# Kernel tuning notes

Hardware: AMD Instinct MI355X
Metric: run time of the kernel (lower is better)

Reference implementation:

```python
import jax, jax.numpy as jnp
import numpy as np

VAR0, VAR1 = 0.1, 0.2
THRESHOLD = 0.35
NEGPOS_RATIO = 7
LOW_GT_THRESH = 0.2  # match() filters GT whose best prior IoU < 0.2


def setup_inputs() -> dict:
    key = jax.random.key(0)
    ks = jax.random.split(key, 8)
    B, P, G = 16, 43008, 128
    loc_data = jax.random.normal(ks[0], (B, P, 4), jnp.float32)
    conf_data = jax.random.normal(ks[1], (B, P, 2), jnp.float32)
    landm_data = jax.random.normal(ks[2], (B, P, 10), jnp.float32)
    # priors in cxcywh form, positive sizes
    pc = jax.random.uniform(ks[3], (P, 2), jnp.float32)
    pwh = jax.random.uniform(ks[4], (P, 2), jnp.float32, minval=0.02, maxval=0.32)
    priors = jnp.concatenate([pc, pwh], axis=1)
    # targets: valid xyxy boxes + 10 landmark coords + label (face=1)
    ctr = jax.random.uniform(ks[5], (B, G, 2), jnp.float32, minval=0.2, maxval=0.8)
    wh = jax.random.uniform(ks[6], (B, G, 2), jnp.float32, minval=0.05, maxval=0.3)
    boxes = jnp.concatenate([ctr - wh / 2, ctr + wh / 2], axis=-1)
    landms = jax.random.uniform(ks[7], (B, G, 10), jnp.float32)
    labels = jnp.ones((B, G, 1), jnp.float32)
    targets = jnp.concatenate([boxes, landms, labels], axis=-1)
    return {"loc_data": loc_data, "conf_data": conf_data, "landm_data": landm_data,
            "priors": priors, "targets": targets}


def point_form(priors):
    return jnp.concatenate([priors[:, :2] - priors[:, 2:] / 2,
                            priors[:, :2] + priors[:, 2:] / 2], axis=1)


def jaccard(a, b):  # a: [G,4] xyxy, b: [P,4] xyxy -> [G,P]
    lt = jnp.maximum(a[:, None, :2], b[None, :, :2])
    rb = jnp.minimum(a[:, None, 2:], b[None, :, 2:])
    wh = jnp.clip(rb - lt, 0.0)
    inter = wh[..., 0] * wh[..., 1]
    area_a = (a[:, 2] - a[:, 0]) * (a[:, 3] - a[:, 1])
    area_b = (b[:, 2] - b[:, 0]) * (b[:, 3] - b[:, 1])
    return inter / (area_a[:, None] + area_b[None, :] - inter)


def encode(matched, priors):  # matched xyxy [P,4], priors cxcywh [P,4]
    g_cxcy = (matched[:, :2] + matched[:, 2:]) / 2 - priors[:, :2]
    g_cxcy = g_cxcy / (VAR0 * priors[:, 2:])
    g_wh = jnp.log((matched[:, 2:] - matched[:, :2]) / priors[:, 2:]) / VAR1
    return jnp.concatenate([g_cxcy, g_wh], axis=1)


def encode_landm(matched, priors):  # matched [P,10], priors [P,4]
    m = matched.reshape(-1, 5, 2)
    g = (m - priors[:, None, :2]) / (VAR0 * priors[:, None, 2:])
    return g.reshape(-1, 10)


def match_one(truths, labels, landms, priors):
    G = truths.shape[0]
    overlaps = jaccard(truths, point_form(priors))  # [G, P]
    best_prior_overlap = overlaps.max(axis=1)       # [G]
    best_prior_idx = overlaps.argmax(axis=1)        # [G]
    valid = best_prior_overlap >= LOW_GT_THRESH
    any_valid = jnp.any(valid)
    best_truth_overlap = overlaps.max(axis=0)       # [P]
    best_truth_idx = overlaps.argmax(axis=0)        # [P]
    # index_fill_(0, best_prior_idx_filter, 2): ensure each valid GT keeps its best prior
    fill_val = jnp.where(valid, 2.0, best_truth_overlap[best_prior_idx])
    best_truth_overlap = best_truth_overlap.at[best_prior_idx].set(fill_val)
    # best_truth_idx[best_prior_idx[j]] = j for all j
    best_truth_idx = best_truth_idx.at[best_prior_idx].set(jnp.arange(G))
    matches = truths[best_truth_idx]                       # [P,4]
    conf = labels[best_truth_idx].astype(jnp.int32)        # [P]
    conf = jnp.where(best_truth_overlap < THRESHOLD, 0, conf)
    conf = jnp.where(any_valid, conf, 0)  # no valid GT -> all background
    loc = encode(matches, priors)
    landm = encode_landm(landms[best_truth_idx], priors)
    return loc, conf, landm


def smooth_l1(x):
    ax = jnp.abs(x)
    return jnp.where(ax < 1.0, 0.5 * ax * ax, ax - 0.5)


def reference(loc_data, conf_data, landm_data, priors, targets):
    truths = targets[..., :4]
    landms = targets[..., 4:14]
    labels = targets[..., 14]
    loc_t, conf_t, landm_t = jax.vmap(
        lambda t, l, lm: match_one(t, l, lm, priors))(truths, labels, landms)

    # landmark loss over positives
    pos1 = conf_t > 0
    N1 = jnp.maximum(pos1.sum().astype(jnp.float32), 1.0)
    loss_landm = jnp.sum(smooth_l1(landm_data - landm_t) * pos1[..., None])

    # localization loss over positives
    pos = conf_t != 0
    num_pos = pos.sum(axis=1, keepdims=True)  # [B,1]
    loss_l = jnp.sum(smooth_l1(loc_data - loc_t) * pos[..., None])

    # hard negative mining on per-prior CE loss
    lse = jax.scipy.special.logsumexp(conf_data, axis=-1)  # [B,P]
    gathered = jnp.take_along_axis(conf_data, conf_t[..., None], axis=-1)[..., 0]
    ce_all = lse - gathered                                # [B,P] per-prior CE
    mine = jnp.where(pos, 0.0, ce_all)
    loss_idx = jnp.argsort(-mine, axis=1)
    idx_rank = jnp.argsort(loss_idx, axis=1)
    num_neg = jnp.clip(NEGPOS_RATIO * num_pos, None, pos.shape[1] - 1)
    neg = idx_rank < num_neg
    sel = pos | neg
    loss_c = jnp.sum(jnp.where(sel, ce_all, 0.0))

    N = jnp.maximum(num_pos.sum().astype(jnp.float32), 1.0)
    return loss_l / N, loss_c / N, loss_landm / N1
```

## Files before the change

kernel.cpp:

```cpp
#include <hip/hip_runtime.h>
#include <stdint.h>


#define GC 8
#define PPI 4

__device__ __forceinline__ float sl1(float x) {
  float a = fabsf(x);
  return a < 1.f ? 0.5f * a * a : a - 0.5f;
}

__device__ __forceinline__ double dwave(double v) {
#pragma unroll
  for (int o = 32; o; o >>= 1) v += __shfl_down(v, o);
  return v;
}

__global__ __launch_bounds__(256) void k_mm(
    const float* __restrict__ priors, const float* __restrict__ targets,
    const float* __restrict__ loc, const float* __restrict__ conf,
    const float* __restrict__ lm, float* __restrict__ bto,
    int* __restrict__ bti, unsigned long long* __restrict__ bp,
    float* __restrict__ mine, unsigned* __restrict__ ghist,
    double* __restrict__ pll, double* __restrict__ pllm,
    double* __restrict__ plc, double* __restrict__ msum,
    int* __restrict__ pnp, int P, int G, int NIOU, int PTI, int NGC, int PC) {
  int tid = threadIdx.x;
  __shared__ char smem[16384];
  __shared__ float4 sgt[128];
  __shared__ float sga[128];

  if ((int)blockIdx.x < NIOU) {
    float* st = (float*)smem;
    double* rs = (double*)(smem + 7680);
    int* ri = (int*)(smem + 7808);
    unsigned* hist = (unsigned*)(smem + 8192);
    int b = blockIdx.x / PTI, tile = blockIdx.x % PTI;
    int base = tile * (256 * PPI);
    for (int i = tid; i < G * 15; i += 256)
      st[i] = targets[(size_t)b * G * 15 + i];
    for (int g = tid; g < G; g += 256) {
      const float* t = targets + ((size_t)b * G + g) * 15;
      float x1 = t[0], y1 = t[1], x2 = t[2], y2 = t[3];
      sgt[g] = make_float4(x1, y1, x2, y2);
      sga[g] = (x2 - x1) * (y2 - y1);
    }
    for (int i = tid; i < 1024; i += 256) hist[i] = 0;
    __syncthreads();

    float px1[PPI], py1[PPI], px2[PPI], py2[PPI], pa[PPI];
    float bi[PPI], sb[PPI];
    int bidx[PPI];
#pragma unroll
    for (int k = 0; k < PPI; ++k) {
      int p = base + tid + k * 256;
      int pl = p < P ? p : P - 1;
      float4 pr = ((const float4*)priors)[pl];
      px1[k] = pr.x - pr.z * 0.5f; py1[k] = pr.y - pr.w * 0.5f;
      px2[k] = pr.x + pr.z * 0.5f; py2[k] = pr.y + pr.w * 0.5f;
      pa[k] = pr.z * pr.w;
      bi[k] = 0.f; sb[k] = 1.f; bidx[k] = 0;
    }

#define IOU_BODY(T, A, GG)                                                 \
  {                                                                        \
    float iw = fminf(T.z, px2[k]) - fmaxf(T.x, px1[k]);                    \
    float ih = fminf(T.w, py2[k]) - fmaxf(T.y, py1[k]);                    \
    float inter = fmaxf(iw, 0.f) * ih;                                     \
    float S = A + pa[k];                                                   \
    if (inter * sb[k] > bi[k] * S) { bi[k] = inter; sb[k] = S; bidx[k] = GG; } \
  }
    for (int g = 0; g < G; g += 4) {
      float4 T0 = sgt[g], T1 = sgt[g + 1], T2 = sgt[g + 2], T3 = sgt[g + 3];
      float A0 = sga[g], A1 = sga[g + 1], A2 = sga[g + 2], A3 = sga[g + 3];
#pragma unroll
      for (int k = 0; k < PPI; ++k) {
        IOU_BODY(T0, A0, g)
        IOU_BODY(T1, A1, g + 1)
        IOU_BODY(T2, A2, g + 2)
        IOU_BODY(T3, A3, g + 3)
      }
    }
#undef IOU_BODY

    double ll = 0, llm = 0, lc = 0, ms = 0;
    int np = 0;
#pragma unroll
    for (int k = 0; k < PPI; ++k) {
      int p = base + tid + k * 256;
      if (p < P) {
        size_t idx = (size_t)b * P + p;
        float ov = bi[k] / (sb[k] - bi[k]);
        int ti = bidx[k];
        bto[idx] = ov;
        bti[idx] = ti;
        bool pos = ov >= 0.35f;
        float2 c = ((const float2*)conf)[idx];
        float mx = fmaxf(c.x, c.y);
        float dd = fabsf(c.x - c.y);
        float lse = mx + logf(1.f + expf(-dd));
        float ce = lse - (pos ? c.y : c.x);
        float mv = pos ? 0.f : ce;
        mine[idx] = mv;
        atomicAdd(&hist[__float_as_uint(mv) >> 21], 1u);
        ms += (double)mv;
        if (pos) {
          np++;
          lc += (double)ce;
          float4 pr = ((const float4*)priors)[p];
          const float* t = st + ti * 15;
          float rz = 1.f / pr.z, rw = 1.f / pr.w;
          float rdx = 10.f * rz, rdy = 10.f * rw;
          float gx = ((t[0] + t[2]) * 0.5f - pr.x) * rdx;
          float gy = ((t[1] + t[3]) * 0.5f - pr.y) * rdy;
          float gw = logf((t[2] - t[0]) * rz) * 5.0f;
          float gh = logf((t[3] - t[1]) * rw) * 5.0f;
          float4 ld = ((const float4*)loc)[idx];
          ll += (double)(sl1(ld.x - gx) + sl1(ld.y - gy) + sl1(ld.z - gw) +
                         sl1(ld.w - gh));
          const float2* lmd = (const float2*)lm + idx * 5;
          float s = 0.f;
#pragma unroll
          for (int j = 0; j < 5; ++j) {
            float2 lv = lmd[j];
            float ex = (t[4 + 2 * j] - pr.x) * rdx;
            float ey = (t[5 + 2 * j] - pr.y) * rdy;
            s += sl1(lv.x - ex) + sl1(lv.y - ey);
          }
          llm += (double)s;
        }
      }
    }

    ll = dwave(ll); llm = dwave(llm); lc = dwave(lc); ms = dwave(ms);
#pragma unroll
    for (int o = 32; o; o >>= 1) np += __shfl_down(np, o);
    int lane = tid & 63, wid = tid >> 6;
    if (lane == 0) {
      rs[wid] = ll; rs[4 + wid] = llm; rs[8 + wid] = lc; rs[12 + wid] = ms;
      ri[wid] = np;
    }
    __syncthreads();
    if (tid == 0) {
      pll[blockIdx.x] = rs[0] + rs[1] + rs[2] + rs[3];
      pllm[blockIdx.x] = rs[4] + rs[5] + rs[6] + rs[7];
      plc[blockIdx.x] = rs[8] + rs[9] + rs[10] + rs[11];
      msum[blockIdx.x] = rs[12] + rs[13] + rs[14] + rs[15];
      pnp[blockIdx.x] = ri[0] + ri[1] + ri[2] + ri[3];
    }
    for (int i = tid; i < 1024; i += 256) {
      unsigned c = hist[i];
      if (c) atomicAdd(&ghist[b * 1024 + i], c);
    }
  } else {
    unsigned long long* sred = (unsigned long long*)smem;
    int bc = blockIdx.x - NIOU;
    int pc = bc % PC;
    int gcb = (bc / PC) % NGC;
    int b = bc / (PC * NGC);
    int g0 = gcb * GC;

    if (tid < GC) {
      int g = g0 + tid;
      float4 v = make_float4(0.f, 0.f, 0.f, 0.f);
      if (g < G) {
        const float* t = targets + ((size_t)b * G + g) * 15;
        v = make_float4(t[0], t[1], t[2], t[3]);
      }
      sgt[tid] = v;
    }
    __syncthreads();

    float gx1[GC], gy1[GC], gx2[GC], gy2[GC], ga[GC];
#pragma unroll
    for (int j = 0; j < GC; ++j) {
      float4 T = sgt[j];
      gx1[j] = T.x; gy1[j] = T.y; gx2[j] = T.z; gy2[j] = T.w;
      ga[j] = (T.z - T.x) * (T.w - T.y);
    }

    int chunk = (P + PC - 1) / PC;
    int ps = pc * chunk;
    int pe = ps + chunk; if (pe > P) pe = P;
    int count = pe - ps;

    float bi[GC], sb[GC];
    unsigned bpp[GC];
#pragma unroll
    for (int j = 0; j < GC; ++j) { bi[j] = 0.f; sb[j] = 1.f; bpp[j] = (unsigned)(ps + tid); }

#define BP_BODY(X1, Y1, X2, Y2, AR, PP)                                     \
  {                                                                         \
    float iw = fminf(gx2[j], X2) - fmaxf(gx1[j], X1);                       \
    float ih = fminf(gy2[j], Y2) - fmaxf(gy1[j], Y1);                       \
    float inter = fmaxf(iw, 0.f) * ih;                                      \
    float S = ga[j] + AR;                                                   \
    if (inter * sb[j] > bi[j] * S) { bi[j] = inter; sb[j] = S; bpp[j] = (unsigned)PP; } \
  }
    for (int i = tid; i < count; i += 1024) {
      int p0 = ps + i;
      int i1 = i + 256, i2 = i + 512, i3 = i + 768;
      int p1 = (i1 < count) ? ps + i1 : p0;
      int p2 = (i2 < count) ? ps + i2 : p0;
      int p3 = (i3 < count) ? ps + i3 : p0;
      float4 q0 = ((const float4*)priors)[p0];
      float4 q1 = ((const float4*)priors)[p1];
      float4 q2 = ((const float4*)priors)[p2];
      float4 q3 = ((const float4*)priors)[p3];
      float ax1 = q0.x - q0.z * 0.5f, ay1 = q0.y - q0.w * 0.5f;
      float ax2 = q0.x + q0.z * 0.5f, ay2 = q0.y + q0.w * 0.5f;
      float aa = q0.z * q0.w;
      float bx1 = q1.x - q1.z * 0.5f, by1 = q1.y - q1.w * 0.5f;
      float bx2 = q1.x + q1.z * 0.5f, by2 = q1.y + q1.w * 0.5f;
      float ba = q1.z * q1.w;
      float cx1 = q2.x - q2.z * 0.5f, cy1 = q2.y - q2.w * 0.5f;
      float cx2 = q2.x + q2.z * 0.5f, cy2 = q2.y + q2.w * 0.5f;
      float ca = q2.z * q2.w;
      float dx1 = q3.x - q3.z * 0.5f, dy1 = q3.y - q3.w * 0.5f;
      float dx2 = q3.x + q3.z * 0.5f, dy2 = q3.y + q3.w * 0.5f;
      float da = q3.z * q3.w;
#pragma unroll
      for (int j = 0; j < GC; ++j) {
        BP_BODY(ax1, ay1, ax2, ay2, aa, p0)
        BP_BODY(bx1, by1, bx2, by2, ba, p1)
        BP_BODY(cx1, cy1, cx2, cy2, ca, p2)
        BP_BODY(dx1, dy1, dx2, dy2, da, p3)
      }
    }
#undef BP_BODY

#pragma unroll
    for (int j = 0; j < GC; ++j) {
      float iou = bi[j] / (sb[j] - bi[j]);
      unsigned long long pk =
          ((unsigned long long)__float_as_uint(iou) << 32) | (unsigned)(~bpp[j]);
      sred[j * 256 + tid] = pk;
    }
    __syncthreads();
    {
      int j = tid >> 5, s = tid & 31;
      unsigned long long m = sred[j * 256 + s];
#pragma unroll
      for (int t = 1; t < 8; ++t) {
        unsigned long long v = sred[j * 256 + s + t * 32];
        if (v > m) m = v;
      }
      __syncthreads();
      sred[j * 256 + s] = m;
    }
    __syncthreads();
    if (tid < GC) {
      unsigned long long m = sred[tid * 256];
      for (int s = 1; s < 32; ++s) {
        unsigned long long v = sred[tid * 256 + s];
        if (v > m) m = v;
      }
      int g = g0 + tid;
      if (g < G) atomicMax(&bp[(size_t)b * G + g], m);
    }
  }
}

__global__ __launch_bounds__(1024) void k_selfix(
    const unsigned long long* __restrict__ bp, const float* __restrict__ bto,
    const int* __restrict__ bti, const float* __restrict__ conf,
    const float* __restrict__ loc, const float* __restrict__ lm,
    const float* __restrict__ priors, const float* __restrict__ targets,
    float* __restrict__ mine, unsigned* __restrict__ ghist,
    const int* __restrict__ pnp, const double* __restrict__ msum,
    const double* __restrict__ pll, const double* __restrict__ pllm,
    const double* __restrict__ plc, int* __restrict__ num_pos,
    double* __restrict__ pllb, double* __restrict__ pllmb,
    double* __restrict__ plcb, int* __restrict__ selstate,
    double* __restrict__ pfs_b, int P, int G, int PTI) {
  int b = blockIdx.x, tid = threadIdx.x;
  __shared__ unsigned spp[128];
  __shared__ double rs[16 * 5];
  __shared__ int ris[16];
  __shared__ unsigned S[1024];
  __shared__ double sdel[4];
  __shared__ int sdnp, sav, smode;
  __shared__ long long sk;

  double dll = 0, dllm = 0, dlc = 0, dms = 0;
  int dnp = 0;
  unsigned pp = 0;
  bool valid = false;
  if (tid < G) {
    unsigned long long m = bp[(size_t)b * G + tid];
    pp = ~(unsigned)m;
    float val = __uint_as_float((unsigned)(m >> 32));
    spp[tid] = pp;
    valid = val >= 0.2f;
  }
  int av = __syncthreads_or((tid < G && valid) ? 1 : 0);
  bool win = false;
  if (tid < G) {
    win = true;
    for (int g2 = tid + 1; g2 < G; ++g2)
      if (spp[g2] == pp) { win = false; break; }
  }
  if (win) {
    size_t idx = (size_t)b * P + pp;
    float ov_o = bto[idx];
    int ti_o = bti[idx];
    float ov_n = valid ? 2.0f : ov_o;
    int ti_n = tid;
    bool pos_o = ov_o >= 0.35f, pos_n = ov_n >= 0.35f;

    float2 c = ((const float2*)conf)[idx];
    float mx = fmaxf(c.x, c.y);
    float dd = fabsf(c.x - c.y);
    float lse = mx + logf(1.f + expf(-dd));
    float ce_o = lse - (pos_o ? c.y : c.x);
    float ce_n = lse - (pos_n ? c.y : c.x);
    float mv_o = mine[idx];
    float mv_n = pos_n ? 0.f : ce_n;
    if (mv_n != mv_o) {
      mine[idx] = mv_n;
      atomicSub(&ghist[b * 1024 + (__float_as_uint(mv_o) >> 21)], 1u);
      atomicAdd(&ghist[b * 1024 + (__float_as_uint(mv_n) >> 21)], 1u);
    }
    dms = (double)mv_n - (double)mv_o;
    dnp = (pos_n ? 1 : 0) - (pos_o ? 1 : 0);
    dlc = (pos_n ? (double)ce_n : 0.0) - (pos_o ? (double)ce_o : 0.0);

    if (pos_o || pos_n) {
      float4 pr = ((const float4*)priors)[pp];
      float rz = 1.f / pr.z, rw = 1.f / pr.w;
      float rdx = 10.f * rz, rdy = 10.f * rw;
      float4 ld = ((const float4*)loc)[idx];
      const float2* lmd = (const float2*)lm + idx * 5;
      float2 lv[5];
#pragma unroll
      for (int j = 0; j < 5; ++j) lv[j] = lmd[j];
      for (int pass = 0; pass < 2; ++pass) {
        bool act = pass ? pos_n : pos_o;
        int ti = pass ? ti_n : ti_o;
        if (!act) continue;
        const float* t = targets + ((size_t)b * G + ti) * 15;
        float gx = ((t[0] + t[2]) * 0.5f - pr.x) * rdx;
        float gy = ((t[1] + t[3]) * 0.5f - pr.y) * rdy;
        float gw = logf((t[2] - t[0]) * rz) * 5.0f;
        float gh = logf((t[3] - t[1]) * rw) * 5.0f;
        double l = (double)(sl1(ld.x - gx) + sl1(ld.y - gy) +
                            sl1(ld.z - gw) + sl1(ld.w - gh));
        float s = 0.f;
#pragma unroll
        for (int j = 0; j < 5; ++j) {
          float ex = (t[4 + 2 * j] - pr.x) * rdx;
          float ey = (t[5 + 2 * j] - pr.y) * rdy;
          s += sl1(lv[j].x - ex) + sl1(lv[j].y - ey);
        }
        if (pass) { dll += l; dllm += (double)s; }
        else { dll -= l; dllm -= (double)s; }
      }
    }
  }
  dll = dwave(dll); dllm = dwave(dllm); dlc = dwave(dlc); dms = dwave(dms);
#pragma unroll
  for (int o = 32; o; o >>= 1) dnp += __shfl_down(dnp, o);
  int lane = tid & 63, wid = tid >> 6;
  if (lane == 0) {
    rs[wid] = dll; rs[16 + wid] = dllm; rs[32 + wid] = dlc; rs[48 + wid] = dms;
    ris[wid] = dnp;
  }
  __syncthreads();
  if (tid == 0) {
    double a = 0, c2 = 0, d2 = 0, m2 = 0;
    int n2 = 0;
    for (int i = 0; i < 16; ++i) {
      a += rs[i]; c2 += rs[16 + i]; d2 += rs[32 + i]; m2 += rs[48 + i];
      n2 += ris[i];
    }
    sdel[0] = a; sdel[1] = c2; sdel[2] = d2; sdel[3] = m2;
    sdnp = n2; sav = av;
  }
  __syncthreads();

  double a = 0, cc = 0, d = 0, ms = 0;
  int n = 0;
  for (int i = tid; i < PTI; i += 1024) {
    int ix = b * PTI + i;
    a += pll[ix]; cc += pllm[ix]; d += plc[ix]; ms += msum[ix]; n += pnp[ix];
  }
  a = dwave(a); cc = dwave(cc); d = dwave(d); ms = dwave(ms);
#pragma unroll
  for (int o = 32; o; o >>= 1) n += __shfl_down(n, o);
  if (lane == 0) {
    rs[wid] = a; rs[16 + wid] = cc; rs[32 + wid] = d; rs[48 + wid] = ms;
    ris[wid] = n;
  }
  __syncthreads();
  if (tid == 0) {
    double A = 0, C = 0, D = 0, MS = 0;
    int npos = 0;
    for (int i = 0; i < 16; ++i) {
      A += rs[i]; C += rs[16 + i]; D += rs[32 + i]; MS += rs[48 + i];
      npos += ris[i];
    }
    A += sdel[0]; C += sdel[1]; D += sdel[2]; MS += sdel[3];
    npos += sdnp;
    if (!sav) { A = 0; C = 0; D = 0; npos = 0; }
    num_pos[b] = npos;
    pllb[b] = A; pllmb[b] = C; plcb[b] = D;
    long long k = 7LL * (long long)npos;
    long long cap = P - 1;
    int md = 1;
    if (k <= 0) { pfs_b[b] = 0.0; selstate[2 * b] = -1; md = 0; }
    else if (k >= cap) { pfs_b[b] = MS; selstate[2 * b] = -1; md = 0; }
    smode = md; sk = k;
  }
  __syncthreads();
  if (!smode) return;
  long long k = sk;

  S[tid] = ghist[b * 1024 + tid];
  __syncthreads();
  for (int off = 1; off < 1024; off <<= 1) {
    unsigned add = (tid + off < 1024) ? S[tid + off] : 0;
    __syncthreads();
    S[tid] += add;
    __syncthreads();
  }
  int cnt_ = __syncthreads_count((long long)S[tid] >= k);
  int seg = cnt_ - 1;
  if (tid == seg) {
    long long cum = (seg + 1 < 1024) ? (long long)S[seg + 1] : 0;
    selstate[2 * b] = seg;
    selstate[2 * b + 1] = (int)(k - cum);
  }
}

__global__ __launch_bounds__(256) void k_compact(
    const int* __restrict__ selstate, const float* __restrict__ mine,
    float* __restrict__ cbuf, unsigned* __restrict__ cntb,
    double* __restrict__ part_hi, int P, int NCC) {
  int b = blockIdx.x / NCC, blk = blockIdx.x % NCC;
  int t = selstate[2 * b];
  if (t < 0) return;
  __shared__ unsigned lcnt, lbase;
  __shared__ double sa[4];
  if (threadIdx.x == 0) lcnt = 0;
  __syncthreads();
  int base = blk * 1024;
  double acc = 0;
  float keep[4];
  int nk = 0;
  for (int i = threadIdx.x; i < 1024; i += 256) {
    int p = base + i;
    if (p < P) {
      unsigned bb = __float_as_uint(mine[(size_t)b * P + p]);
      int bin = (int)(bb >> 21);
      if (bin > t) acc += (double)__uint_as_float(bb);
      else if (bin == t) keep[nk++] = __uint_as_float(bb);
    }
  }
  unsigned myoff = nk ? atomicAdd(&lcnt, (unsigned)nk) : 0u;
  __syncthreads();
  if (threadIdx.x == 0) lbase = lcnt ? atomicAdd(&cntb[b], lcnt) : 0u;
  __syncthreads();
  unsigned wb = lbase + myoff;
  for (int j = 0; j < nk; ++j) cbuf[(size_t)b * P + wb + j] = keep[j];
  acc = dwave(acc);
  int lane = threadIdx.x & 63, wid = threadIdx.x >> 6;
  if (lane == 0) sa[wid] = acc;
  __syncthreads();
  if (threadIdx.x == 0)
    part_hi[(size_t)b * NCC + blk] = sa[0] + sa[1] + sa[2] + sa[3];
}

__global__ __launch_bounds__(1024) void k_sel2(
    const int* __restrict__ selstate, const float* __restrict__ cbuf,
    const unsigned* __restrict__ cntb, const double* __restrict__ part_hi,
    double* __restrict__ pfs_b, int P, int NCC) {
  int b = blockIdx.x, tid = threadIdx.x;
  int t = selstate[2 * b];
  if (t < 0) return;
  long long k1 = (long long)selstate[2 * b + 1];
  int n = (int)cntb[b];
  const float* row = cbuf + (size_t)b * P;
  __shared__ unsigned hs[2048];
  __shared__ unsigned S[1024];
  __shared__ double rs[16];
  __shared__ int spf21, sk2;
  __shared__ unsigned stb;
  __shared__ double stie;

  hs[tid] = 0; hs[tid + 1024] = 0;
  __syncthreads();
  for (int i = tid; i < n; i += 1024) {
    unsigned bb = __float_as_uint(row[i]);
    atomicAdd(&hs[(bb >> 10) & 2047], 1u);
  }
  __syncthreads();
  {
    unsigned h0 = hs[tid * 2], h1v = hs[tid * 2 + 1];
    S[tid] = h0 + h1v;
    __syncthreads();
    for (int off = 1; off < 1024; off <<= 1) {
      unsigned add = (tid + off < 1024) ? S[tid + off] : 0;
      __syncthreads();
      S[tid] += add;
      __syncthreads();
    }
    int cnt_ = __syncthreads_count((long long)S[tid] >= k1);
    int seg = cnt_ - 1;
    if (tid == seg) {
      long long cum = (seg + 1 < 1024) ? (long long)S[seg + 1] : 0;
      int bin = seg * 2;
      if (cum + h1v >= k1) bin = seg * 2 + 1;
      else cum += h1v;
      spf21 = (t << 11) | bin;
      sk2 = (int)(k1 - cum);
    }
  }
  __syncthreads();
  int pf21 = spf21;

  hs[tid] = 0;
  __syncthreads();
  for (int i = tid; i < n; i += 1024) {
    unsigned bb = __float_as_uint(row[i]);
    if ((int)(bb >> 10) == pf21) atomicAdd(&hs[bb & 1023], 1u);
  }
  __syncthreads();
  {
    S[tid] = hs[tid];
    __syncthreads();
    for (int off = 1; off < 1024; off <<= 1) {
      unsigned add = (tid + off < 1024) ? S[tid + off] : 0;
      __syncthreads();
      S[tid] += add;
      __syncthreads();
    }
    long long kk = (long long)sk2;
    int cnt_ = __syncthreads_count((long long)S[tid] >= kk);
    int seg = cnt_ - 1;
    if (tid == seg) {
      long long cum = (seg + 1 < 1024) ? (long long)S[seg + 1] : 0;
      unsigned tb = ((unsigned)pf21 << 10) | (unsigned)seg;
      stb = tb;
      stie = (double)(kk - cum) * (double)__uint_as_float(tb);
    }
  }
  __syncthreads();

  unsigned tb = stb;
  double v = 0.0;
  for (int i = tid; i < n; i += 1024) {
    unsigned bb = __float_as_uint(row[i]);
    if (bb > tb) v += (double)__uint_as_float(bb);
  }
  v = dwave(v);
  int lane = tid & 63, wid = tid >> 6;
  if (lane == 0) rs[wid] = v;
  __syncthreads();
  if (tid == 0) {
    double hi = 0;
    for (int j = 0; j < NCC; ++j) hi += part_hi[(size_t)b * NCC + j];
    double tot = 0;
    for (int i = 0; i < 16; ++i) tot += rs[i];
    pfs_b[b] = hi + tot + stie;
  }
}

__global__ void k_fin(const double* __restrict__ pllb,
                      const double* __restrict__ pllmb,
                      const double* __restrict__ plcb,
                      const double* __restrict__ pfs_b,
                      const int* __restrict__ num_pos, float* __restrict__ out,
                      int B) {
  if (threadIdx.x == 0) {
    double A = 0, C = 0, D = 0, F = 0, N = 0;
    for (int i = 0; i < B; ++i) {
      A += pllb[i]; C += pllmb[i]; D += plcb[i]; F += pfs_b[i];
      N += (double)num_pos[i];
    }
    if (N < 1.0) N = 1.0;
    out[0] = (float)(A / N);
    out[1] = (float)((D + F) / N);
    out[2] = (float)(C / N);
  }
}

extern "C" void kernel_launch(void* const* d_in, const int* in_sizes, int n_in,
                              void* d_out, int out_size, void* d_ws,
                              size_t ws_size, hipStream_t stream) {
  const float* loc = (const float*)d_in[0];
  const float* conf = (const float*)d_in[1];
  const float* lm = (const float*)d_in[2];
  const float* priors = (const float*)d_in[3];
  const float* targets = (const float*)d_in[4];

  int P = in_sizes[3] / 4;
  int B = in_sizes[0] / (4 * P);
  int G = in_sizes[4] / (15 * B);
  int PTI = (P + 256 * PPI - 1) / (256 * PPI);
  int NIOU = B * PTI;
  int NGC = (G + GC - 1) / GC;
  int PC = 8;
  int NBP = B * NGC * PC;
  int NCC = (P + 1023) / 1024;

  char* w = (char*)d_ws;
  size_t off = 0;
  unsigned long long* bp = (unsigned long long*)(w + off);
  off += (size_t)B * G * 8;
  unsigned* ghist = (unsigned*)(w + off);
  off += (size_t)B * 1024 * 4;
  unsigned* cntb = (unsigned*)(w + off);
  off += (size_t)B * 4;
  size_t clear_bytes = off;
  off = (off + 255) & ~(size_t)255;
  float* bto = (float*)(w + off);
  off += (size_t)B * P * 4;
  int* bti = (int*)(w + off);
  off += (size_t)B * P * 4;
  float* mine = (float*)(w + off);
  off += (size_t)B * P * 4;
  double* pll = (double*)(w + off);
  off += (size_t)NIOU * 8;
  double* pllm = (double*)(w + off);
  off += (size_t)NIOU * 8;
  double* plc = (double*)(w + off);
  off += (size_t)NIOU * 8;
  double* msum = (double*)(w + off);
  off += (size_t)NIOU * 8;
  int* pnp = (int*)(w + off);
  off += (size_t)NIOU * 4;
  off = (off + 7) & ~(size_t)7;
  double* part_hi = (double*)(w + off);
  off += (size_t)B * NCC * 8;
  double* pllb = (double*)(w + off);
  off += (size_t)B * 8;
  double* pllmb = (double*)(w + off);
  off += (size_t)B * 8;
  double* plcb = (double*)(w + off);
  off += (size_t)B * 8;
  double* pfs_b = (double*)(w + off);
  off += (size_t)B * 8;
  int* selstate = (int*)(w + off);
  off += (size_t)B * 2 * 4;
  int* num_pos = (int*)(w + off);
  off += (size_t)B * 4;

  hipMemsetAsync(d_ws, 0, clear_bytes, stream);

  k_mm<<<NIOU + NBP, 256, 0, stream>>>(priors, targets, loc, conf, lm, bto,
                                       bti, bp, mine, ghist, pll, pllm, plc,
                                       msum, pnp, P, G, NIOU, PTI, NGC, PC);
  k_selfix<<<B, 1024, 0, stream>>>(bp, bto, bti, conf, loc, lm, priors,
                                   targets, mine, ghist, pnp, msum, pll, pllm,
                                   plc, num_pos, pllb, pllmb, plcb, selstate,
                                   pfs_b, P, G, PTI);
  k_compact<<<B * NCC, 256, 0, stream>>>(selstate, mine, bto, cntb, part_hi,
                                         P, NCC);
  k_sel2<<<B, 1024, 0, stream>>>(selstate, bto, cntb, part_hi, pfs_b, P, NCC);
  k_fin<<<1, 64, 0, stream>>>(pllb, pllmb, plcb, pfs_b, num_pos,
                              (float*)d_out, B);
}
```

Baseline: 181.2 us.

## Fuse selection, compaction, radix select and final reduction into one tail kernel

Merges k_selfix, k_compact, k_sel2 and k_fin into a single per-batch kernel (B blocks of 1024 threads). The threshold-bin compaction now runs inside that block, using a shared atomic counter. The final cross-batch reduction uses global double atomics plus a last-block-done counter. The Hillis-Steele suffix scans are replaced with a wave-shuffle based block scan. This removes three kernel launches and their inter-kernel gaps, but the compaction pass over P elements now runs on only 16 blocks, which lowers parallelism for that stage.

After: 179.2 us. No clear change (-1.1%).

```diff
diff --git a/kernel.cpp b/kernel.cpp
--- a/kernel.cpp
+++ b/kernel.cpp
@@ -14,6 +14,33 @@
 #pragma unroll
   for (int o = 32; o; o >>= 1) v += __shfl_down(v, o);
   return v;
+}
+
+__device__ __forceinline__ unsigned bsufscan(unsigned x, unsigned* S,
+                                             unsigned* wt, int tid) {
+  int lane = tid & 63, wid = tid >> 6;
+  unsigned v = x;
+#pragma unroll
+  for (int o = 1; o < 64; o <<= 1) {
+    unsigned u = __shfl_down(v, o);
+    if (lane + o < 64) v += u;
+  }
+  if (lane == 0) wt[wid] = v;
+  __syncthreads();
+  if (wid == 0) {
+    unsigned tv = (lane < 16) ? wt[lane] : 0;
+#pragma unroll
+    for (int o = 1; o < 16; o <<= 1) {
+      unsigned u = __shfl_down(tv, o);
+      if (lane + o < 64) tv += u;
+    }
+    if (lane < 16) wt[lane] = tv;
+  }
+  __syncthreads();
+  unsigned Sv = v + ((wid < 15) ? wt[wid + 1] : 0u);
+  S[tid] = Sv;
+  __syncthreads();
+  return Sv;
 }
 
 __global__ __launch_bounds__(256) void k_mm(
@@ -261,26 +288,35 @@
   }
 }
 
-__global__ __launch_bounds__(1024) void k_selfix(
-    const unsigned long long* __restrict__ bp, const float* __restrict__ bto,
+__global__ __launch_bounds__(1024) void k_tail2(
+    const unsigned long long* __restrict__ bp, float* __restrict__ bto,
     const int* __restrict__ bti, const float* __restrict__ conf,
     const float* __restrict__ loc, const float* __restrict__ lm,
     const float* __restrict__ priors, const float* __restrict__ targets,
     float* __restrict__ mine, unsigned* __restrict__ ghist,
     const int* __restrict__ pnp, const double* __restrict__ msum,
     const double* __restrict__ pll, const double* __restrict__ pllm,
-    const double* __restrict__ plc, int* __restrict__ num_pos,
-    double* __restrict__ pllb, double* __restrict__ pllmb,
-    double* __restrict__ plcb, int* __restrict__ selstate,
-    double* __restrict__ pfs_b, int P, int G, int PTI) {
+    const double* __restrict__ plc, double* __restrict__ gacc,
+    int* __restrict__ gnp, unsigned* __restrict__ done,
+    float* __restrict__ out, int P, int G, int PTI, int B) {
   int b = blockIdx.x, tid = threadIdx.x;
+  int lane = tid & 63, wid = tid >> 6;
   __shared__ unsigned spp[128];
   __shared__ double rs[16 * 5];
   __shared__ int ris[16];
   __shared__ unsigned S[1024];
+  __shared__ unsigned hs[2048];
+  __shared__ unsigned wt[16];
   __shared__ double sdel[4];
   __shared__ int sdnp, sav, smode;
   __shared__ long long sk;
+  __shared__ double sA, sC, sD;
+  __shared__ int snpos;
+  __shared__ int st_, sk1_;
+  __shared__ unsigned lcnt;
+  __shared__ int spf21, sk2;
+  __shared__ unsigned stb;
+  __shared__ double stie;
 
   double dll = 0, dllm = 0, dlc = 0, dms = 0;
   int dnp = 0;
@@ -360,7 +396,6 @@
   dll = dwave(dll); dllm = dwave(dllm); dlc = dwave(dlc); dms = dwave(dms);
 #pragma unroll
   for (int o = 32; o; o >>= 1) dnp += __shfl_down(dnp, o);
-  int lane = tid & 63, wid = tid >> 6;
   if (lane == 0) {
     rs[wid] = dll; rs[16 + wid] = dllm; rs[32 + wid] = dlc; rs[48 + wid] = dms;
     ris[wid] = dnp;
@@ -392,6 +427,7 @@
     ris[wid] = n;
   }
   __syncthreads();
+  double Fv = 0.0;
   if (tid == 0) {
     double A = 0, C = 0, D = 0, MS = 0;
     int npos = 0;
@@ -402,185 +438,138 @@
     A += sdel[0]; C += sdel[1]; D += sdel[2]; MS += sdel[3];
     npos += sdnp;
     if (!sav) { A = 0; C = 0; D = 0; npos = 0; }
-    num_pos[b] = npos;
-    pllb[b] = A; pllmb[b] = C; plcb[b] = D;
+    sA = A; sC = C; sD = D; snpos = npos;
     long long k = 7LL * (long long)npos;
     long long cap = P - 1;
     int md = 1;
-    if (k <= 0) { pfs_b[b] = 0.0; selstate[2 * b] = -1; md = 0; }
-    else if (k >= cap) { pfs_b[b] = MS; selstate[2 * b] = -1; md = 0; }
+    if (k <= 0) { Fv = 0.0; md = 0; }
+    else if (k >= cap) { Fv = MS; md = 0; }
     smode = md; sk = k;
   }
   __syncthreads();
-  if (!smode) return;
-  long long k = sk;
-
-  S[tid] = ghist[b * 1024 + tid];
-  __syncthreads();
-  for (int off = 1; off < 1024; off <<= 1) {
-    unsigned add = (tid + off < 1024) ? S[tid + off] : 0;
-    __syncthreads();
-    S[tid] += add;
-    __syncthreads();
-  }
-  int cnt_ = __syncthreads_count((long long)S[tid] >= k);
-  int seg = cnt_ - 1;
-  if (tid == seg) {
-    long long cum = (seg + 1 < 1024) ? (long long)S[seg + 1] : 0;
-    selstate[2 * b] = seg;
-    selstate[2 * b + 1] = (int)(k - cum);
-  }
-}
-
-__global__ __launch_bounds__(256) void k_compact(
-    const int* __restrict__ selstate, const float* __restrict__ mine,
-    float* __restrict__ cbuf, unsigned* __restrict__ cntb,
-    double* __restrict__ part_hi, int P, int NCC) {
-  int b = blockIdx.x / NCC, blk = blockIdx.x % NCC;
-  int t = selstate[2 * b];
-  if (t < 0) return;
-  __shared__ unsigned lcnt, lbase;
-  __shared__ double sa[4];
-  if (threadIdx.x == 0) lcnt = 0;
-  __syncthreads();
-  int base = blk * 1024;
-  double acc = 0;
-  float keep[4];
-  int nk = 0;
-  for (int i = threadIdx.x; i < 1024; i += 256) {
-    int p = base + i;
-    if (p < P) {
-      unsigned bb = __float_as_uint(mine[(size_t)b * P + p]);
-      int bin = (int)(bb >> 21);
-      if (bin > t) acc += (double)__uint_as_float(bb);
-      else if (bin == t) keep[nk++] = __uint_as_float(bb);
-    }
-  }
-  unsigned myoff = nk ? atomicAdd(&lcnt, (unsigned)nk) : 0u;
-  __syncthreads();
-  if (threadIdx.x == 0) lbase = lcnt ? atomicAdd(&cntb[b], lcnt) : 0u;
-  __syncthreads();
-  unsigned wb = lbase + myoff;
-  for (int j = 0; j < nk; ++j) cbuf[(size_t)b * P + wb + j] = keep[j];
-  acc = dwave(acc);
-  int lane = threadIdx.x & 63, wid = threadIdx.x >> 6;
-  if (lane == 0) sa[wid] = acc;
-  __syncthreads();
-  if (threadIdx.x == 0)
-    part_hi[(size_t)b * NCC + blk] = sa[0] + sa[1] + sa[2] + sa[3];
-}
-
-__global__ __launch_bounds__(1024) void k_sel2(
-    const int* __restrict__ selstate, const float* __restrict__ cbuf,
-    const unsigned* __restrict__ cntb, const double* __restrict__ part_hi,
-    double* __restrict__ pfs_b, int P, int NCC) {
-  int b = blockIdx.x, tid = threadIdx.x;
-  int t = selstate[2 * b];
-  if (t < 0) return;
-  long long k1 = (long long)selstate[2 * b + 1];
-  int n = (int)cntb[b];
-  const float* row = cbuf + (size_t)b * P;
-  __shared__ unsigned hs[2048];
-  __shared__ unsigned S[1024];
-  __shared__ double rs[16];
-  __shared__ int spf21, sk2;
-  __shared__ unsigned stb;
-  __shared__ double stie;
-
-  hs[tid] = 0; hs[tid + 1024] = 0;
-  __syncthreads();
-  for (int i = tid; i < n; i += 1024) {
-    unsigned bb = __float_as_uint(row[i]);
-    atomicAdd(&hs[(bb >> 10) & 2047], 1u);
-  }
-  __syncthreads();
-  {
-    unsigned h0 = hs[tid * 2], h1v = hs[tid * 2 + 1];
-    S[tid] = h0 + h1v;
-    __syncthreads();
-    for (int off = 1; off < 1024; off <<= 1) {
-      unsigned add = (tid + off < 1024) ? S[tid + off] : 0;
-      __syncthreads();
-      S[tid] += add;
-      __syncthreads();
-    }
-    int cnt_ = __syncthreads_count((long long)S[tid] >= k1);
-    int seg = cnt_ - 1;
-    if (tid == seg) {
-      long long cum = (seg + 1 < 1024) ? (long long)S[seg + 1] : 0;
-      int bin = seg * 2;
-      if (cum + h1v >= k1) bin = seg * 2 + 1;
-      else cum += h1v;
-      spf21 = (t << 11) | bin;
-      sk2 = (int)(k1 - cum);
-    }
-  }
-  __syncthreads();
-  int pf21 = spf21;
-
-  hs[tid] = 0;
-  __syncthreads();
-  for (int i = tid; i < n; i += 1024) {
-    unsigned bb = __float_as_uint(row[i]);
-    if ((int)(bb >> 10) == pf21) atomicAdd(&hs[bb & 1023], 1u);
-  }
-  __syncthreads();
-  {
-    S[tid] = hs[tid];
-    __syncthreads();
-    for (int off = 1; off < 1024; off <<= 1) {
-      unsigned add = (tid + off < 1024) ? S[tid + off] : 0;
-      __syncthreads();
-      S[tid] += add;
-      __syncthreads();
-    }
-    long long kk = (long long)sk2;
-    int cnt_ = __syncthreads_count((long long)S[tid] >= kk);
-    int seg = cnt_ - 1;
-    if (tid == seg) {
-      long long cum = (seg + 1 < 1024) ? (long long)S[seg + 1] : 0;
-      unsigned tb = ((unsigned)pf21 << 10) | (unsigned)seg;
-      stb = tb;
-      stie = (double)(kk - cum) * (double)__uint_as_float(tb);
-    }
-  }
-  __syncthreads();
-
-  unsigned tb = stb;
-  double v = 0.0;
-  for (int i = tid; i < n; i += 1024) {
-    unsigned bb = __float_as_uint(row[i]);
-    if (bb > tb) v += (double)__uint_as_float(bb);
-  }
-  v = dwave(v);
-  int lane = tid & 63, wid = tid >> 6;
-  if (lane == 0) rs[wid] = v;
-  __syncthreads();
+
+  if (smode) {
+    long long k = sk;
+    {
+      unsigned x = ghist[b * 1024 + tid];
+      unsigned Sv = bsufscan(x, S, wt, tid);
+      int cnt_ = __syncthreads_count((long long)Sv >= k);
+      int seg = cnt_ - 1;
+      if (tid == seg) {
+        long long cum = (seg + 1 < 1024) ? (long long)S[seg + 1] : 0;
+        st_ = seg;
+        sk1_ = (int)(k - cum);
+      }
+      if (tid == 0) lcnt = 0;
+    }
+    __syncthreads();
+    int t = st_;
+    long long k1 = (long long)sk1_;
+
+    const float* mrow = mine + (size_t)b * P;
+    float* crow = bto + (size_t)b * P;
+    double acc = 0;
+    for (int base0 = 0; base0 < P; base0 += 4096) {
+#pragma unroll
+      for (int j = 0; j < 4; ++j) {
+        int p = base0 + tid + j * 1024;
+        if (p < P) {
+          unsigned bb = __float_as_uint(mrow[p]);
+          int bin = (int)(bb >> 21);
+          if (bin > t) acc += (double)__uint_as_float(bb);
+          else if (bin == t) {
+            unsigned pos = atomicAdd(&lcnt, 1u);
+            crow[pos] = __uint_as_float(bb);
+          }
+        }
+      }
+    }
+    acc = dwave(acc);
+    if (lane == 0) rs[wid] = acc;
+    __syncthreads();
+    int nn = (int)lcnt;
+
+    hs[tid] = 0; hs[tid + 1024] = 0;
+    __syncthreads();
+    for (int i = tid; i < nn; i += 1024) {
+      unsigned bb = __float_as_uint(crow[i]);
+      atomicAdd(&hs[(bb >> 10) & 2047], 1u);
+    }
+    __syncthreads();
+    {
+      unsigned h0 = hs[tid * 2], h1v = hs[tid * 2 + 1];
+      unsigned Sv = bsufscan(h0 + h1v, S, wt, tid);
+      int cnt_ = __syncthreads_count((long long)Sv >= k1);
+      int seg = cnt_ - 1;
+      if (tid == seg) {
+        long long cum = (seg + 1 < 1024) ? (long long)S[seg + 1] : 0;
+        int bin = seg * 2;
+        if (cum + h1v >= k1) bin = seg * 2 + 1;
+        else cum += h1v;
+        spf21 = (t << 11) | bin;
+        sk2 = (int)(k1 - cum);
+      }
+    }
+    __syncthreads();
+    int pf21 = spf21;
+
+    hs[tid] = 0;
+    __syncthreads();
+    for (int i = tid; i < nn; i += 1024) {
+      unsigned bb = __float_as_uint(crow[i]);
+      if ((int)(bb >> 10) == pf21) atomicAdd(&hs[bb & 1023], 1u);
+    }
+    __syncthreads();
+    {
+      unsigned Sv = bsufscan(hs[tid], S, wt, tid);
+      long long kk = (long long)sk2;
+      int cnt_ = __syncthreads_count((long long)Sv >= kk);
+      int seg = cnt_ - 1;
+      if (tid == seg) {
+        long long cum = (seg + 1 < 1024) ? (long long)S[seg + 1] : 0;
+        unsigned tb = ((unsigned)pf21 << 10) | (unsigned)seg;
+        stb = tb;
+        stie = (double)(kk - cum) * (double)__uint_as_float(tb);
+      }
+    }
+    __syncthreads();
+
+    unsigned tb = stb;
+    double v = 0.0;
+    for (int i = tid; i < nn; i += 1024) {
+      unsigned bb = __float_as_uint(crow[i]);
+      if (bb > tb) v += (double)__uint_as_float(bb);
+    }
+    v = dwave(v);
+    if (lane == 0) rs[16 + wid] = v;
+    __syncthreads();
+    if (tid == 0) {
+      double hi = 0, vt = 0;
+      for (int i = 0; i < 16; ++i) { hi += rs[i]; vt += rs[16 + i]; }
+      Fv = hi + vt + stie;
+    }
+  }
+
   if (tid == 0) {
-    double hi = 0;
-    for (int j = 0; j < NCC; ++j) hi += part_hi[(size_t)b * NCC + j];
-    double tot = 0;
-    for (int i = 0; i < 16; ++i) tot += rs[i];
-    pfs_b[b] = hi + tot + stie;
-  }
-}
-
-__global__ void k_fin(const double* __restrict__ pllb,
-                      const double* __restrict__ pllmb,
-                      const double* __restrict__ plcb,
-                      const double* __restrict__ pfs_b,
-                      const int* __restrict__ num_pos, float* __restrict__ out,
-                      int B) {
-  if (threadIdx.x == 0) {
-    double A = 0, C = 0, D = 0, F = 0, N = 0;
-    for (int i = 0; i < B; ++i) {
-      A += pllb[i]; C += pllmb[i]; D += plcb[i]; F += pfs_b[i];
-      N += (double)num_pos[i];
-    }
-    if (N < 1.0) N = 1.0;
-    out[0] = (float)(A / N);
-    out[1] = (float)((D + F) / N);
-    out[2] = (float)(C / N);
+    atomicAdd(&gacc[0], sA);
+    atomicAdd(&gacc[1], sC);
+    atomicAdd(&gacc[2], sD);
+    atomicAdd(&gacc[3], Fv);
+    atomicAdd(gnp, snpos);
+    __threadfence();
+    unsigned old = atomicAdd(done, 1u);
+    if (old == (unsigned)B - 1) {
+      __threadfence();
+      double A = atomicAdd(&gacc[0], 0.0);
+      double C = atomicAdd(&gacc[1], 0.0);
+      double D = atomicAdd(&gacc[2], 0.0);
+      double F = atomicAdd(&gacc[3], 0.0);
+      int N = atomicAdd(gnp, 0);
+      double Nd = N < 1 ? 1.0 : (double)N;
+      out[0] = (float)(A / Nd);
+      out[1] = (float)((D + F) / Nd);
+      out[2] = (float)(C / Nd);
+    }
   }
 }
 
@@ -601,7 +590,6 @@
   int NGC = (G + GC - 1) / GC;
   int PC = 8;
   int NBP = B * NGC * PC;
-  int NCC = (P + 1023) / 1024;
 
   char* w = (char*)d_ws;
   size_t off = 0;
@@ -609,8 +597,12 @@
   off += (size_t)B * G * 8;
   unsigned* ghist = (unsigned*)(w + off);
   off += (size_t)B * 1024 * 4;
-  unsigned* cntb = (unsigned*)(w + off);
-  off += (size_t)B * 4;
+  double* gacc = (double*)(w + off);
+  off += 4 * 8;
+  int* gnp = (int*)(w + off);
+  off += 4;
+  unsigned* done = (unsigned*)(w + off);
+  off += 4;
   size_t clear_bytes = off;
   off = (off + 255) & ~(size_t)255;
   float* bto = (float*)(w + off);
@@ -629,34 +621,14 @@
   off += (size_t)NIOU * 8;
   int* pnp = (int*)(w + off);
   off += (size_t)NIOU * 4;
-  off = (off + 7) & ~(size_t)7;
-  double* part_hi = (double*)(w + off);
-  off += (size_t)B * NCC * 8;
-  double* pllb = (double*)(w + off);
-  off += (size_t)B * 8;
-  double* pllmb = (double*)(w + off);
-  off += (size_t)B * 8;
-  double* plcb = (double*)(w + off);
-  off += (size_t)B * 8;
-  double* pfs_b = (double*)(w + off);
-  off += (size_t)B * 8;
-  int* selstate = (int*)(w + off);
-  off += (size_t)B * 2 * 4;
-  int* num_pos = (int*)(w + off);
-  off += (size_t)B * 4;
 
   hipMemsetAsync(d_ws, 0, clear_bytes, stream);
 
   k_mm<<<NIOU + NBP, 256, 0, stream>>>(priors, targets, loc, conf, lm, bto,
                                        bti, bp, mine, ghist, pll, pllm, plc,
                                        msum, pnp, P, G, NIOU, PTI, NGC, PC);
-  k_selfix<<<B, 1024, 0, stream>>>(bp, bto, bti, conf, loc, lm, priors,
-                                   targets, mine, ghist, pnp, msum, pll, pllm,
-                                   plc, num_pos, pllb, pllmb, plcb, selstate,
-                                   pfs_b, P, G, PTI);
-  k_compact<<<B * NCC, 256, 0, stream>>>(selstate, mine, bto, cntb, part_hi,
-                                         P, NCC);
-  k_sel2<<<B, 1024, 0, stream>>>(selstate, bto, cntb, part_hi, pfs_b, P, NCC);
-  k_fin<<<1, 64, 0, stream>>>(pllb, pllmb, plcb, pfs_b, num_pos,
-                              (float*)d_out, B);
+  k_tail2<<<B, 1024, 0, stream>>>(bp, bto, bti, conf, loc, lm, priors,
+                                  targets, mine, ghist, pnp, msum, pll, pllm,
+                                  plc, gacc, gnp, done, (float*)d_out, P, G,
+                                  PTI, B);
 }
```
